# Kernel tuning notes

Hardware: AMD Instinct MI355X
Metric: run time of the kernel (lower is better)

Reference implementation:

```python
import jax, jax.numpy as jnp
import numpy as np

N_NODES = 100000
N_EDGES = 1200000
D = 64
NUM_LAYERS = 3
K = 3


def setup_inputs() -> dict:
    key = jax.random.key(0)
    k1, k2, k3, k4 = jax.random.split(key, 4)
    x = jax.random.normal(k1, (N_NODES, D), dtype=jnp.float32)
    edge_index = jax.random.randint(k2, (2, N_EDGES), 0, N_NODES, dtype=jnp.int64)
    # per-layer Chebyshev linear weights [L, K, in, out] and single bias per layer [L, out]
    W = jax.random.normal(k3, (NUM_LAYERS, K, D, D), dtype=jnp.float32) / np.sqrt(D)
    b = jax.random.normal(k4, (NUM_LAYERS, D), dtype=jnp.float32) * 0.01
    return {"x": x, "edge_index": edge_index, "W": W, "b": b}


def _cheb_norm(edge_index, n_nodes):
    # PyG ChebConv.__norm__ with sym normalization, lambda_max=2.0, no edge weights:
    # scaled Laplacian L_hat = -D^{-1/2} A D^{-1/2} (diagonal cancels to 0).
    row, col = edge_index[0], edge_index[1]
    deg = jax.ops.segment_sum(jnp.ones_like(row, dtype=jnp.float32), row,
                              num_segments=n_nodes)
    deg_inv_sqrt = jnp.where(deg > 0, jax.lax.rsqrt(jnp.maximum(deg, 1.0)), 0.0)
    norm = -deg_inv_sqrt[row] * deg_inv_sqrt[col]  # [E]
    return norm


def _propagate(h, src, dst, norm, n_nodes):
    # out[i] = sum_{e: dst_e = i} norm_e * h[src_e]
    msgs = norm[:, None] * h[src]  # [E, D]
    return jax.ops.segment_sum(msgs, dst, num_segments=n_nodes)


def _cheb_conv(h, src, dst, norm, Wl, bl, n_nodes):
    # Tx_0 = h; Tx_1 = L_hat h; Tx_k = 2 L_hat Tx_{k-1} - Tx_{k-2}
    Tx0 = h
    out = Tx0 @ Wl[0]
    Tx1 = _propagate(Tx0, src, dst, norm, n_nodes)
    out = out + Tx1 @ Wl[1]
    for k in range(2, K):
        Tx2 = 2.0 * _propagate(Tx1, src, dst, norm, n_nodes) - Tx0
        out = out + Tx2 @ Wl[k]
        Tx0, Tx1 = Tx1, Tx2
    return out + bl


def reference(x, edge_index, W, b) -> jnp.ndarray:
    n_nodes = x.shape[0]
    src, dst = edge_index[0], edge_index[1]  # flow source_to_target: j=src, i=dst
    norm = _cheb_norm(edge_index, n_nodes)
    # input_dim == hidden_dim -> no input projection; h_prev starts as x
    h_prev = x
    for i in range(NUM_LAYERS):
        inp = x if i == 0 else h_prev
        out = _cheb_conv(inp, src, dst, norm, W[i], b[i], n_nodes)
        if i > 0:
            out = out + h_prev
        h_prev = jax.nn.relu(out)  # dropout identity in eval mode
    return h_prev
```

## Files before the change

kernel.cpp:

```cpp
#include <hip/hip_runtime.h>

#define N_NODES 100000
#define N_EDGES 1200000
#define D 64
#define NUM_LAYERS 3

#define NB 196
#define BSZ 512
#define NPAD (NB * BSZ)
#define CHUNK 4096
#define NCHUNK ((N_EDGES + CHUNK - 1) / CHUNK)
#define ZROW N_NODES
#define BSLACK 3592

typedef unsigned int uint;
typedef unsigned short u16;

using short8 = __attribute__((ext_vector_type(8))) short;
using f32x4  = __attribute__((ext_vector_type(4))) float;

static __device__ __forceinline__ float b2f(u16 u) {
    return __uint_as_float(((uint)u) << 16);
}
static __device__ __forceinline__ u16 f2b(float f) {
    uint u = __float_as_uint(f);
    return (u16)((u + 0x7FFFu + ((u >> 16) & 1u)) >> 16);
}

__global__ __launch_bounds__(256) void hist_kernel(const int* __restrict__ src,
        const int* __restrict__ dst, int* __restrict__ cnt2, int E) {
    __shared__ int hD[NB], hS[NB];
    for (int i = threadIdx.x; i < NB; i += 256) { hD[i] = 0; hS[i] = 0; }
    __syncthreads();
    int i = blockIdx.x * 256 + threadIdx.x;
    int stride = gridDim.x * 256;
    for (; i < E; i += stride) {
        atomicAdd(&hD[((unsigned)dst[i]) >> 9], 1);
        atomicAdd(&hS[((unsigned)src[i]) >> 9], 1);
    }
    __syncthreads();
    for (int i2 = threadIdx.x; i2 < NB; i2 += 256) {
        if (hD[i2]) atomicAdd(&cnt2[i2], hD[i2]);
        if (hS[i2]) atomicAdd(&cnt2[NB + i2], hS[i2]);
    }
}

__global__ __launch_bounds__(256) void scanb_kernel(const int* __restrict__ cnt2,
        int* __restrict__ base2, int* __restrict__ curs2) {
    __shared__ int buf[256];
    int t = threadIdx.x;
    for (int arr = 0; arr < 2; ++arr) {
        int v = (t < NB) ? cnt2[arr * NB + t] : 0;
        buf[t] = v;
        __syncthreads();
        for (int off = 1; off < 256; off <<= 1) {
            int u = (t >= off) ? buf[t - off] : 0;
            __syncthreads();
            buf[t] += u;
            __syncthreads();
        }
        int excl = buf[t] - v;
        if (t < NB) {
            base2[arr * (NB + 1) + t] = excl;
            curs2[arr * NB + t] = excl;
        }
        if (t == NB - 1) base2[arr * (NB + 1) + NB] = buf[t];
        __syncthreads();
    }
}

__global__ __launch_bounds__(256) void part_kernel(const int* __restrict__ src,
        const int* __restrict__ dst, int* __restrict__ cursD, int* __restrict__ cursS,
        int* __restrict__ dstPart, u16* __restrict__ srcPart, int E) {
    __shared__ int eS[CHUNK], eT[CHUNK];
    __shared__ int hD[NB], hS[NB], bD[NB], bS[NB];
    int e0 = blockIdx.x * CHUNK;
    int n = min(CHUNK, E - e0);
    for (int i = threadIdx.x; i < NB; i += 256) { hD[i] = 0; hS[i] = 0; }
    for (int i = threadIdx.x; i < n; i += 256) { eS[i] = src[e0 + i]; eT[i] = dst[e0 + i]; }
    __syncthreads();
    for (int i = threadIdx.x; i < n; i += 256) {
        atomicAdd(&hD[((unsigned)eT[i]) >> 9], 1);
        atomicAdd(&hS[((unsigned)eS[i]) >> 9], 1);
    }
    __syncthreads();
    for (int i = threadIdx.x; i < NB; i += 256) {
        bD[i] = hD[i] ? atomicAdd(&cursD[i], hD[i]) : 0;
        bS[i] = hS[i] ? atomicAdd(&cursS[i], hS[i]) : 0;
        hD[i] = 0; hS[i] = 0;
    }
    __syncthreads();
    for (int i = threadIdx.x; i < n; i += 256) {
        int s = eS[i], t = eT[i];
        int kb = ((unsigned)t) >> 9;
        int pos = bD[kb] + atomicAdd(&hD[kb], 1);
        dstPart[pos] = ((t & 511) << 20) | s;
        kb = ((unsigned)s) >> 9;
        pos = bS[kb] + atomicAdd(&hS[kb], 1);
        srcPart[pos] = (u16)(s & 511);
    }
}

__global__ __launch_bounds__(256) void csr_kernel(const int* __restrict__ baseD,
        const int* __restrict__ dstPart, int* __restrict__ rowptr,
        int* __restrict__ rowend, int* __restrict__ cv) {
    __shared__ int cnt[BSZ], curs[BSZ], psum[256];
    int b = blockIdx.x, t = threadIdx.x;
    int node0 = b * BSZ;
    int eb = baseD[b], ee = baseD[b + 1];
    int padbase = ((eb + 7) & ~7) + b * BSLACK;
    for (int i = t; i < BSZ; i += 256) cnt[i] = 0;
    __syncthreads();
    for (int e = eb + t; e < ee; e += 256)
        atomicAdd(&cnt[((unsigned)dstPart[e]) >> 20], 1);
    __syncthreads();
    int c0 = cnt[2 * t], c1 = cnt[2 * t + 1];
    int p0 = (c0 + 7) & ~7, p1 = (c1 + 7) & ~7;
    psum[t] = p0 + p1;
    __syncthreads();
    for (int off = 1; off < 256; off <<= 1) {
        int u = (t >= off) ? psum[t - off] : 0;
        __syncthreads();
        psum[t] += u;
        __syncthreads();
    }
    int excl = psum[t] - p0 - p1;
    int start0 = padbase + excl;
    int start1 = start0 + p0;
    curs[2 * t] = start0;
    curs[2 * t + 1] = start1;
    int n0 = node0 + 2 * t;
    if (n0 < N_NODES)     { rowptr[n0]     = start0; rowend[n0]     = start0 + p0; }
    if (n0 + 1 < N_NODES) { rowptr[n0 + 1] = start1; rowend[n0 + 1] = start1 + p1; }
    __syncthreads();
    for (int e = eb + t; e < ee; e += 256) {
        int p = dstPart[e];
        int loc = ((unsigned)p) >> 20;
        int pos = atomicAdd(&curs[loc], 1);
        cv[pos] = p & 0xFFFFF;
    }
    __syncthreads();
    for (int q = c0; q < p0; ++q) cv[start0 + q] = ZROW;
    for (int q = c1; q < p1; ++q) cv[start1 + q] = ZROW;
}

__global__ __launch_bounds__(256) void degs_kernel(const int* __restrict__ baseS,
        const u16* __restrict__ srcPart, float* __restrict__ dinv) {
    __shared__ int cnt[BSZ];
    int b = blockIdx.x, t = threadIdx.x;
    int eb = baseS[b], ee = baseS[b + 1];
    for (int i = t; i < BSZ; i += 256) cnt[i] = 0;
    __syncthreads();
    for (int e = eb + t; e < ee; e += 256)
        atomicAdd(&cnt[srcPart[e]], 1);
    __syncthreads();
    for (int i = t; i < BSZ; i += 256) {
        int node = b * BSZ + i;
        if (node < N_NODES) {
            int d = cnt[i];
            dinv[node] = (d > 0) ? rsqrtf((float)d) : 0.0f;
        }
    }
}

__global__ __launch_bounds__(256) void wprep_kernel(const float* __restrict__ W,
        u16* __restrict__ Wb) {
    int i = blockIdx.x * 256 + threadIdx.x;
    if (i >= 72 * 512) return;
    int j = i & 7;
    int lane = (i >> 3) & 63;
    int fid = i >> 9;
    int ni = fid & 1;
    int t = fid >> 1;
    int kt = t % 6;
    int t2 = t / 6;
    int wn = t2 & 1;
    int l = t2 >> 1;
    int k = kt * 32 + (lane >> 4) * 8 + j;
    int col = wn * 32 + ni * 16 + (lane & 15);
    float v = W[((size_t)l * 192 + k) * 64 + col];
    if (l > 0 && k == col) v += 1.0f;
    Wb[i] = f2b(v);
}

__global__ void zrow_kernel(u16* a, u16* b, u16* c) {
    int i = threadIdx.x;
    if (i >= 192) return;
    u16* buf = (i < 64) ? a : (i < 128) ? b : c;
    buf[(size_t)ZROW * D + (i & 63)] = 0;
}

__global__ __launch_bounds__(256) void cvt_kernel(const float* __restrict__ x,
        const float* __restrict__ dinv, u16* __restrict__ gx, int nvec) {
    int i = blockIdx.x * blockDim.x + threadIdx.x;
    if (i >= nvec) return;
    float4 v = ((const float4*)x)[i];
    float dv = dinv[i >> 4];
    uint2 b;
    b.x = (uint)f2b(v.x * dv) | ((uint)f2b(v.y * dv) << 16);
    b.y = (uint)f2b(v.z * dv) | ((uint)f2b(v.w * dv) << 16);
    ((uint2*)gx)[i] = b;
}

__global__ __launch_bounds__(256) void gather_kernel(const int* __restrict__ rowptr,
        const int* __restrict__ rowend, const int* __restrict__ cv,
        const u16* __restrict__ g, const float* __restrict__ dinv,
        u16* __restrict__ outp, u16* __restrict__ outscaled, int n) {
    int lane = threadIdx.x & 63;
    int node = __builtin_amdgcn_readfirstlane((int)(blockIdx.x * 4) + (threadIdx.x >> 6));
    if (node >= n) return;
    int p = rowptr[node];
    const int pe = rowend[node];
    const int len = pe - p;
    float a0 = 0.f, a1 = 0.f, a2 = 0.f, a3 = 0.f,
          a4 = 0.f, a5 = 0.f, a6 = 0.f, a7 = 0.f;
    if (len == 16) {
        int4 c0 = *(const int4*)(cv + p);
        int4 c1 = *(const int4*)(cv + p + 4);
        int4 c2 = *(const int4*)(cv + p + 8);
        int4 c3 = *(const int4*)(cv + p + 12);
        float v0  = b2f(g[(size_t)c0.x * D + lane]);
        float v1  = b2f(g[(size_t)c0.y * D + lane]);
        float v2  = b2f(g[(size_t)c0.z * D + lane]);
        float v3  = b2f(g[(size_t)c0.w * D + lane]);
        float v4  = b2f(g[(size_t)c1.x * D + lane]);
        float v5  = b2f(g[(size_t)c1.y * D + lane]);
        float v6  = b2f(g[(size_t)c1.z * D + lane]);
        float v7  = b2f(g[(size_t)c1.w * D + lane]);
        float v8  = b2f(g[(size_t)c2.x * D + lane]);
        float v9  = b2f(g[(size_t)c2.y * D + lane]);
        float v10 = b2f(g[(size_t)c2.z * D + lane]);
        float v11 = b2f(g[(size_t)c2.w * D + lane]);
        float v12 = b2f(g[(size_t)c3.x * D + lane]);
        float v13 = b2f(g[(size_t)c3.y * D + lane]);
        float v14 = b2f(g[(size_t)c3.z * D + lane]);
        float v15 = b2f(g[(size_t)c3.w * D + lane]);
        a0 = (v0 + v8);  a1 = (v1 + v9);  a2 = (v2 + v10); a3 = (v3 + v11);
        a4 = (v4 + v12); a5 = (v5 + v13); a6 = (v6 + v14); a7 = (v7 + v15);
    } else if (len > 0) {
        int4 ca = *(const int4*)(cv + p);
        int4 cb = *(const int4*)(cv + p + 4);
        for (;;) {
            int np = p + 8;
            bool more = np < pe;
            int4 na, nb;
            if (more) {
                na = *(const int4*)(cv + np);
                nb = *(const int4*)(cv + np + 4);
            }
            a0 += b2f(g[(size_t)ca.x * D + lane]);
            a1 += b2f(g[(size_t)ca.y * D + lane]);
            a2 += b2f(g[(size_t)ca.z * D + lane]);
            a3 += b2f(g[(size_t)ca.w * D + lane]);
            a4 += b2f(g[(size_t)cb.x * D + lane]);
            a5 += b2f(g[(size_t)cb.y * D + lane]);
            a6 += b2f(g[(size_t)cb.z * D + lane]);
            a7 += b2f(g[(size_t)cb.w * D + lane]);
            if (!more) break;
            ca = na; cb = nb; p = np;
        }
    }
    float dv = dinv[node];
    float v = -dv * (((a0 + a1) + (a2 + a3)) + ((a4 + a5) + (a6 + a7)));
    size_t ob = (size_t)node * D + lane;
    outp[ob] = f2b(v);
    if (outscaled) outscaled[ob] = f2b(dv * v);
}

template<int INPF32>
__global__ __launch_bounds__(256) void cheb_mfma_kernel(
        const float* __restrict__ x,
        const u16* __restrict__ inp,
        const u16* __restrict__ t1, const u16* __restrict__ t2,
        const u16* __restrict__ Wbl,
        const float* __restrict__ bias, const float* __restrict__ dinv,
        u16* __restrict__ outb, u16* __restrict__ goutb, float* __restrict__ outf,
        int writeScaled, int outF32) {
    const int tid = threadIdx.x;
    const int lane = tid & 63;
    const int w = tid >> 6;
    const int wm = w & 1, wn = w >> 1;
    const int l15 = lane & 15;
    const int l4 = lane >> 4;
    const int koff = l4 * 8;

    const int mbase = blockIdx.x * 64 + wm * 32;
    const int nbase = wn * 32;

    short8 Bf[6][2];
#pragma unroll
    for (int kt = 0; kt < 6; ++kt)
#pragma unroll
        for (int ni = 0; ni < 2; ++ni)
            Bf[kt][ni] = *(const short8*)(Wbl + (size_t)(((wn * 6 + kt) * 2) + ni) * 512 + lane * 8);

    short8 T1[2][2], T2[2][2], Fi[2][2];
    float4 Xf[2][2][2];
#pragma unroll
    for (int mi = 0; mi < 2; ++mi) {
        int row = mbase + mi * 16 + l15;
        int rowc = min(row, N_NODES - 1);
#pragma unroll
        for (int half = 0; half < 2; ++half) {
            T1[mi][half] = *(const short8*)(t1 + (size_t)row * 64 + half * 32 + koff);
            T2[mi][half] = *(const short8*)(t2 + (size_t)row * 64 + half * 32 + koff);
            if (INPF32) {
                const float* p = x + (size_t)rowc * 64 + half * 32 + koff;
                Xf[mi][half][0] = *(const float4*)p;
                Xf[mi][half][1] = *(const float4*)(p + 4);
            } else {
                Fi[mi][half] = *(const short8*)(inp + (size_t)row * 64 + half * 32 + koff);
            }
        }
    }

    float bj0 = bias[nbase + l15];
    float bj1 = bias[nbase + 16 + l15];

    f32x4 acc[2][2];
#pragma unroll
    for (int mi = 0; mi < 2; ++mi)
#pragma unroll
        for (int ni = 0; ni < 2; ++ni)
#pragma unroll
            for (int r = 0; r < 4; ++r) acc[mi][ni][r] = 0.0f;

#pragma unroll
    for (int kt = 0; kt < 6; ++kt) {
        short8 Af[2];
#pragma unroll
        for (int mi = 0; mi < 2; ++mi) {
            short8 a;
            if (kt < 2) {
                if (INPF32) {
                    const float* p = (const float*)&Xf[mi][kt][0];
#pragma unroll
                    for (int j = 0; j < 8; ++j) a[j] = (short)f2b(p[j]);
                } else {
                    a = Fi[mi][kt];
                }
            } else if (kt < 4) {
                a = T1[mi][kt - 2];
            } else {
                short8 a2 = T2[mi][kt - 4];
                if (INPF32) {
                    const float* p = (const float*)&Xf[mi][kt - 4][0];
#pragma unroll
                    for (int j = 0; j < 8; ++j)
                        a[j] = (short)f2b(fmaf(2.0f, b2f((u16)a2[j]), -p[j]));
                } else {
                    short8 ai = Fi[mi][kt - 4];
#pragma unroll
                    for (int j = 0; j < 8; ++j)
                        a[j] = (short)f2b(fmaf(2.0f, b2f((u16)a2[j]), -b2f((u16)ai[j])));
                }
            }
            Af[mi] = a;
        }
#pragma unroll
        for (int mi = 0; mi < 2; ++mi)
#pragma unroll
            for (int ni = 0; ni < 2; ++ni)
                acc[mi][ni] = __builtin_amdgcn_mfma_f32_16x16x32_bf16(
                    Af[mi], Bf[kt][ni], acc[mi][ni], 0, 0, 0);
    }

    float4 dvv[2];
    if (writeScaled) {
#pragma unroll
        for (int mi = 0; mi < 2; ++mi)
            dvv[mi] = *(const float4*)(dinv + mbase + mi * 16 + l4 * 4);
    }
#pragma unroll
    for (int mi = 0; mi < 2; ++mi)
#pragma unroll
        for (int r = 0; r < 4; ++r) {
            int node = mbase + mi * 16 + l4 * 4 + r;
            if (node >= N_NODES) continue;
#pragma unroll
            for (int ni = 0; ni < 2; ++ni) {
                int col = nbase + ni * 16 + l15;
                size_t o = (size_t)node * 64 + col;
                float v = acc[mi][ni][r] + (ni ? bj1 : bj0);
                v = fmaxf(v, 0.0f);
                if (outF32) {
                    outf[o] = v;
                } else {
                    outb[o] = f2b(v);
                    if (writeScaled) {
                        float dv = ((const float*)&dvv[mi])[r];
                        goutb[o] = f2b(v * dv);
                    }
                }
            }
        }
}

extern "C" void kernel_launch(void* const* d_in, const int* in_sizes, int n_in,
                              void* d_out, int out_size, void* d_ws, size_t ws_size,
                              hipStream_t stream) {
    const float* x = (const float*)d_in[0];
    const int* ei = (const int*)d_in[1];
    const float* W = (const float*)d_in[2];
    const float* b = (const float*)d_in[3];
    float* out = (float*)d_out;

    const int* src = ei;
    const int* dst = ei + N_EDGES;

    const size_t NDP = (size_t)NPAD * D;
    const size_t CVSZ = (size_t)N_EDGES + 72 + (size_t)NB * BSLACK;

    char* w = (char*)d_ws;
    int*   cnt2   = (int*)w;        w += (size_t)512 * 4;
    int*   base2  = (int*)w;        w += (size_t)512 * 4;
    int*   curs2  = (int*)w;        w += (size_t)512 * 4;
    int*   rowptr = (int*)w;        w += (size_t)NPAD * 4;
    int*   rowend = (int*)w;        w += (size_t)NPAD * 4;
    float* dinv   = (float*)w;      w += (size_t)NPAD * 4;
    u16*   Wb     = (u16*)w;        w += (size_t)72 * 512 * 2;
    int*   cv     = (int*)w;        w += ((CVSZ + 63) & ~(size_t)63) * 4;
    u16*   gx     = (u16*)w;        w += NDP * 2;
    u16*   h      = (u16*)w;        w += NDP * 2;
    u16*   gh     = (u16*)w;        w += NDP * 2;
    u16*   t1     = (u16*)w;        w += NDP * 2;
    u16*   gt1    = (u16*)w;        w += NDP * 2;
    u16*   t2     = (u16*)w;        w += NDP * 2;
    int*   dstPart = (int*)gt1;
    u16*   srcPart = (u16*)t2;

    int* baseD = base2;
    int* baseS = base2 + (NB + 1);
    int* cursD = curs2;
    int* cursS = curs2 + NB;

    hipMemsetAsync(cnt2, 0, (size_t)(2 * NB) * 4, stream);
    hist_kernel<<<304, 256, 0, stream>>>(src, dst, cnt2, N_EDGES);
    scanb_kernel<<<1, 256, 0, stream>>>(cnt2, base2, curs2);
    part_kernel<<<NCHUNK, 256, 0, stream>>>(src, dst, cursD, cursS, dstPart, srcPart, N_EDGES);
    csr_kernel<<<NB, 256, 0, stream>>>(baseD, dstPart, rowptr, rowend, cv);
    degs_kernel<<<NB, 256, 0, stream>>>(baseS, srcPart, dinv);
    wprep_kernel<<<144, 256, 0, stream>>>(W, Wb);
    zrow_kernel<<<1, 256, 0, stream>>>(gx, gh, gt1);
    cvt_kernel<<<(int)(((size_t)N_NODES * D / 4 + 255) / 256), 256, 0, stream>>>(
        x, dinv, gx, (int)((size_t)N_NODES * D / 4));

    const int gatherBlocks = (N_NODES + 3) / 4;
    const int chebBlocks = NPAD / 64;

    for (int l = 0; l < NUM_LAYERS; ++l) {
        const u16* gin = (l == 0) ? gx : gh;
        gather_kernel<<<gatherBlocks, 256, 0, stream>>>(rowptr, rowend, cv, gin, dinv, t1, gt1, N_NODES);
        gather_kernel<<<gatherBlocks, 256, 0, stream>>>(rowptr, rowend, cv, gt1, dinv, t2, (u16*)0, N_NODES);

        int last = (l == NUM_LAYERS - 1);
        const u16* Wbl = Wb + (size_t)l * 24 * 512;
        const float* bl = b + (size_t)l * D;
        if (l == 0) {
            cheb_mfma_kernel<1><<<chebBlocks, 256, 0, stream>>>(
                x, h, t1, t2, Wbl, bl, dinv, h, gh, out, !last, last);
        } else {
            cheb_mfma_kernel<0><<<chebBlocks, 256, 0, stream>>>(
                x, h, t1, t2, Wbl, bl, dinv, h, gh, out, !last, last);
        }
    }
}
```

Measured before the change: 336.0 us.

## Split gathered feature buffers into two 32-column halves for cache-local gathers

Scaled bf16 feature buffers are stored as two separate half-width planes (32 columns each), and the gather kernel now uses twice as many blocks, each handling one half. Within a wave, four 16-lane groups each load a 4-byte pair for a different neighbor, then reduce across groups with shuffles. The goal is to halve the gather working set per pass so it fits better in L2/MALL and to issue wider per-lane loads. The cost is that index lists are read twice, shuffle reductions are added, and the writers (cvt, cheb MFMA output, zrow) must use the new split layout.

```diff
diff --git a/kernel.cpp b/kernel.cpp
--- a/kernel.cpp
+++ b/kernel.cpp
@@ -12,6 +12,7 @@
 #define NCHUNK ((N_EDGES + CHUNK - 1) / CHUNK)
 #define ZROW N_NODES
 #define BSLACK 3592
+#define HSZ ((size_t)NPAD * 32)
 
 typedef unsigned int uint;
 typedef unsigned short u16;
@@ -25,6 +26,12 @@
 static __device__ __forceinline__ u16 f2b(float f) {
     uint u = __float_as_uint(f);
     return (u16)((u + 0x7FFFu + ((u >> 16) & 1u)) >> 16);
+}
+static __device__ __forceinline__ float blo(uint v) {
+    return __uint_as_float(v << 16);
+}
+static __device__ __forceinline__ float bhi(uint v) {
+    return __uint_as_float(v & 0xFFFF0000u);
 }
 
 __global__ __launch_bounds__(256) void hist_kernel(const int* __restrict__ src,
@@ -187,84 +194,95 @@
     int i = threadIdx.x;
     if (i >= 192) return;
     u16* buf = (i < 64) ? a : (i < 128) ? b : c;
-    buf[(size_t)ZROW * D + (i & 63)] = 0;
+    int r = i & 63;
+    int q = r >> 5, fl = r & 31;
+    buf[(size_t)q * HSZ + (size_t)ZROW * 32 + fl] = 0;
 }
 
 __global__ __launch_bounds__(256) void cvt_kernel(const float* __restrict__ x,
-        const float* __restrict__ dinv, u16* __restrict__ gx, int nvec) {
+        const float* __restrict__ dinv, u16* __restrict__ gx2, int nvec) {
     int i = blockIdx.x * blockDim.x + threadIdx.x;
     if (i >= nvec) return;
     float4 v = ((const float4*)x)[i];
-    float dv = dinv[i >> 4];
+    int node = i >> 4;
+    int c = (i & 15) * 4;
+    float dv = dinv[node];
     uint2 b;
     b.x = (uint)f2b(v.x * dv) | ((uint)f2b(v.y * dv) << 16);
     b.y = (uint)f2b(v.z * dv) | ((uint)f2b(v.w * dv) << 16);
-    ((uint2*)gx)[i] = b;
+    *(uint2*)(gx2 + (size_t)(c >> 5) * HSZ + (size_t)node * 32 + (c & 31)) = b;
 }
 
 __global__ __launch_bounds__(256) void gather_kernel(const int* __restrict__ rowptr,
         const int* __restrict__ rowend, const int* __restrict__ cv,
-        const u16* __restrict__ g, const float* __restrict__ dinv,
-        u16* __restrict__ outp, u16* __restrict__ outscaled, int n) {
+        const u16* __restrict__ g2, const float* __restrict__ dinv,
+        u16* __restrict__ trow, u16* __restrict__ gq2, int n) {
+    const int G2 = (N_NODES + 3) / 4;
+    int bid = blockIdx.x;
+    int q = (bid >= G2) ? 1 : 0;
+    int nb = q ? bid - G2 : bid;
     int lane = threadIdx.x & 63;
-    int node = __builtin_amdgcn_readfirstlane((int)(blockIdx.x * 4) + (threadIdx.x >> 6));
+    int li = lane & 15;
+    int grp = lane >> 4;
+    int node = __builtin_amdgcn_readfirstlane(nb * 4 + (threadIdx.x >> 6));
     if (node >= n) return;
+    const u16* __restrict__ gq = g2 + (size_t)q * HSZ;
+
     int p = rowptr[node];
     const int pe = rowend[node];
-    const int len = pe - p;
-    float a0 = 0.f, a1 = 0.f, a2 = 0.f, a3 = 0.f,
-          a4 = 0.f, a5 = 0.f, a6 = 0.f, a7 = 0.f;
-    if (len == 16) {
+    float s0 = 0.f, s1 = 0.f;
+
+#define SEL(c) ((grp == 0) ? (c).x : (grp == 1) ? (c).y : (grp == 2) ? (c).z : (c).w)
+#define LD(s) (*(const uint*)(gq + (size_t)(s) * 32 + li * 2))
+    if (pe - p == 16) {
         int4 c0 = *(const int4*)(cv + p);
         int4 c1 = *(const int4*)(cv + p + 4);
         int4 c2 = *(const int4*)(cv + p + 8);
         int4 c3 = *(const int4*)(cv + p + 12);
-        float v0  = b2f(g[(size_t)c0.x * D + lane]);
-        float v1  = b2f(g[(size_t)c0.y * D + lane]);
-        float v2  = b2f(g[(size_t)c0.z * D + lane]);
-        float v3  = b2f(g[(size_t)c0.w * D + lane]);
-        float v4  = b2f(g[(size_t)c1.x * D + lane]);
-        float v5  = b2f(g[(size_t)c1.y * D + lane]);
-        float v6  = b2f(g[(size_t)c1.z * D + lane]);
-        float v7  = b2f(g[(size_t)c1.w * D + lane]);
-        float v8  = b2f(g[(size_t)c2.x * D + lane]);
-        float v9  = b2f(g[(size_t)c2.y * D + lane]);
-        float v10 = b2f(g[(size_t)c2.z * D + lane]);
-        float v11 = b2f(g[(size_t)c2.w * D + lane]);
-        float v12 = b2f(g[(size_t)c3.x * D + lane]);
-        float v13 = b2f(g[(size_t)c3.y * D + lane]);
-        float v14 = b2f(g[(size_t)c3.z * D + lane]);
-        float v15 = b2f(g[(size_t)c3.w * D + lane]);
-        a0 = (v0 + v8);  a1 = (v1 + v9);  a2 = (v2 + v10); a3 = (v3 + v11);
-        a4 = (v4 + v12); a5 = (v5 + v13); a6 = (v6 + v14); a7 = (v7 + v15);
-    } else if (len > 0) {
+        uint v0 = LD(SEL(c0));
+        uint v1 = LD(SEL(c1));
+        uint v2 = LD(SEL(c2));
+        uint v3 = LD(SEL(c3));
+        s0 = (blo(v0) + blo(v1)) + (blo(v2) + blo(v3));
+        s1 = (bhi(v0) + bhi(v1)) + (bhi(v2) + bhi(v3));
+    } else if (pe > p) {
         int4 ca = *(const int4*)(cv + p);
         int4 cb = *(const int4*)(cv + p + 4);
         for (;;) {
             int np = p + 8;
             bool more = np < pe;
-            int4 na, nb;
+            int4 na, nb4;
             if (more) {
-                na = *(const int4*)(cv + np);
-                nb = *(const int4*)(cv + np + 4);
+                na  = *(const int4*)(cv + np);
+                nb4 = *(const int4*)(cv + np + 4);
             }
-            a0 += b2f(g[(size_t)ca.x * D + lane]);
-            a1 += b2f(g[(size_t)ca.y * D + lane]);
-            a2 += b2f(g[(size_t)ca.z * D + lane]);
-            a3 += b2f(g[(size_t)ca.w * D + lane]);
-            a4 += b2f(g[(size_t)cb.x * D + lane]);
-            a5 += b2f(g[(size_t)cb.y * D + lane]);
-            a6 += b2f(g[(size_t)cb.z * D + lane]);
-            a7 += b2f(g[(size_t)cb.w * D + lane]);
+            uint v0 = LD(SEL(ca));
+            uint v1 = LD(SEL(cb));
+            s0 += blo(v0) + blo(v1);
+            s1 += bhi(v0) + bhi(v1);
             if (!more) break;
-            ca = na; cb = nb; p = np;
-        }
-    }
-    float dv = dinv[node];
-    float v = -dv * (((a0 + a1) + (a2 + a3)) + ((a4 + a5) + (a6 + a7)));
-    size_t ob = (size_t)node * D + lane;
-    outp[ob] = f2b(v);
-    if (outscaled) outscaled[ob] = f2b(dv * v);
+            ca = na; cb = nb4; p = np;
+        }
+    }
+#undef LD
+#undef SEL
+
+    s0 += __shfl_xor(s0, 16);
+    s0 += __shfl_xor(s0, 32);
+    s1 += __shfl_xor(s1, 16);
+    s1 += __shfl_xor(s1, 32);
+
+    if (grp == 0) {
+        float dv = dinv[node];
+        float v0 = -dv * s0;
+        float v1 = -dv * s1;
+        uint pk = (uint)f2b(v0) | ((uint)f2b(v1) << 16);
+        *(uint*)(trow + (size_t)node * 64 + q * 32 + li * 2) = pk;
+        if (gq2) {
+            uint pg = (uint)f2b(dv * v0) | ((uint)f2b(dv * v1) << 16);
+            *(uint*)(gq2 + (size_t)q * HSZ + (size_t)node * 32 + li * 2) = pg;
+        }
+    }
 }
 
 template<int INPF32>
@@ -274,7 +292,7 @@
         const u16* __restrict__ t1, const u16* __restrict__ t2,
         const u16* __restrict__ Wbl,
         const float* __restrict__ bias, const float* __restrict__ dinv,
-        u16* __restrict__ outb, u16* __restrict__ goutb, float* __restrict__ outf,
+        u16* __restrict__ outb, u16* __restrict__ goutb2, float* __restrict__ outf,
         int writeScaled, int outF32) {
     const int tid = threadIdx.x;
     const int lane = tid & 63;
@@ -389,7 +407,8 @@
                     outb[o] = f2b(v);
                     if (writeScaled) {
                         float dv = ((const float*)&dvv[mi])[r];
-                        goutb[o] = f2b(v * dv);
+                        goutb2[(size_t)wn * HSZ + (size_t)node * 32 + (col & 31)] =
+                            f2b(v * dv);
                     }
                 }
             }
@@ -445,7 +464,8 @@
     cvt_kernel<<<(int)(((size_t)N_NODES * D / 4 + 255) / 256), 256, 0, stream>>>(
         x, dinv, gx, (int)((size_t)N_NODES * D / 4));
 
-    const int gatherBlocks = (N_NODES + 3) / 4;
+    const int G2 = (N_NODES + 3) / 4;
+    const int gatherBlocks = 2 * G2;
     const int chebBlocks = NPAD / 64;
 
     for (int l = 0; l < NUM_LAYERS; ++l) {
```

Measured after the change: 482.2 us. 43.5% more time.

## Keep Chebyshev features in degree-scaled space to drop dual outputs

Applied to the files above, without the earlier changes.

Stores all intermediate features pre-multiplied by D^{-1/2}, so each gather writes a single scaled output (scaled by -1/deg) instead of both raw and scaled copies. The MFMA kernel reads only scaled buffers and rescales accumulators by sqrt(deg) in the epilogue, which removes the fp32 x load path and the second output write. This cuts memory traffic in the gather and combine kernels. Isolated nodes use a scale of 1 to stay correct, and rescaling bf16 values can change rounding.

```diff
diff --git a/kernel.cpp b/kernel.cpp
--- a/kernel.cpp
+++ b/kernel.cpp
@@ -145,7 +145,8 @@
 }
 
 __global__ __launch_bounds__(256) void degs_kernel(const int* __restrict__ baseS,
-        const u16* __restrict__ srcPart, float* __restrict__ dinv) {
+        const u16* __restrict__ srcPart, float* __restrict__ sArr,
+        float* __restrict__ rsArr, float* __restrict__ mArr) {
     __shared__ int cnt[BSZ];
     int b = blockIdx.x, t = threadIdx.x;
     int eb = baseS[b], ee = baseS[b + 1];
@@ -158,7 +159,10 @@
         int node = b * BSZ + i;
         if (node < N_NODES) {
             int d = cnt[i];
-            dinv[node] = (d > 0) ? rsqrtf((float)d) : 0.0f;
+            float fd = (float)d;
+            sArr[node]  = (d > 0) ? rsqrtf(fd) : 1.0f;
+            rsArr[node] = (d > 0) ? sqrtf(fd) : 1.0f;
+            mArr[node]  = (d > 0) ? (-1.0f / fd) : 0.0f;
         }
     }
 }
@@ -191,21 +195,21 @@
 }
 
 __global__ __launch_bounds__(256) void cvt_kernel(const float* __restrict__ x,
-        const float* __restrict__ dinv, u16* __restrict__ gx, int nvec) {
+        const float* __restrict__ sArr, u16* __restrict__ g0, int nvec) {
     int i = blockIdx.x * blockDim.x + threadIdx.x;
     if (i >= nvec) return;
     float4 v = ((const float4*)x)[i];
-    float dv = dinv[i >> 4];
+    float dv = sArr[i >> 4];
     uint2 b;
     b.x = (uint)f2b(v.x * dv) | ((uint)f2b(v.y * dv) << 16);
     b.y = (uint)f2b(v.z * dv) | ((uint)f2b(v.w * dv) << 16);
-    ((uint2*)gx)[i] = b;
+    ((uint2*)g0)[i] = b;
 }
 
 __global__ __launch_bounds__(256) void gather_kernel(const int* __restrict__ rowptr,
         const int* __restrict__ rowend, const int* __restrict__ cv,
-        const u16* __restrict__ g, const float* __restrict__ dinv,
-        u16* __restrict__ outp, u16* __restrict__ outscaled, int n) {
+        const u16* __restrict__ g, const float* __restrict__ mArr,
+        u16* __restrict__ outg, int n) {
     int lane = threadIdx.x & 63;
     int node = __builtin_amdgcn_readfirstlane((int)(blockIdx.x * 4) + (threadIdx.x >> 6));
     if (node >= n) return;
@@ -260,22 +264,16 @@
             ca = na; cb = nb; p = np;
         }
     }
-    float dv = dinv[node];
-    float v = -dv * (((a0 + a1) + (a2 + a3)) + ((a4 + a5) + (a6 + a7)));
-    size_t ob = (size_t)node * D + lane;
-    outp[ob] = f2b(v);
-    if (outscaled) outscaled[ob] = f2b(dv * v);
-}
-
-template<int INPF32>
+    float val = mArr[node] * (((a0 + a1) + (a2 + a3)) + ((a4 + a5) + (a6 + a7)));
+    outg[(size_t)node * D + lane] = f2b(val);
+}
+
 __global__ __launch_bounds__(256) void cheb_mfma_kernel(
-        const float* __restrict__ x,
-        const u16* __restrict__ inp,
-        const u16* __restrict__ t1, const u16* __restrict__ t2,
-        const u16* __restrict__ Wbl,
-        const float* __restrict__ bias, const float* __restrict__ dinv,
-        u16* __restrict__ outb, u16* __restrict__ goutb, float* __restrict__ outf,
-        int writeScaled, int outF32) {
+        const u16* __restrict__ gin, const u16* __restrict__ gt1,
+        const u16* __restrict__ gt2, const u16* __restrict__ Wbl,
+        const float* __restrict__ bias, const float* __restrict__ rsArr,
+        const float* __restrict__ sArr,
+        u16* __restrict__ outg, float* __restrict__ outf, int last) {
     const int tid = threadIdx.x;
     const int lane = tid & 63;
     const int w = tid >> 6;
@@ -294,23 +292,16 @@
         for (int ni = 0; ni < 2; ++ni)
             Bf[kt][ni] = *(const short8*)(Wbl + (size_t)(((wn * 6 + kt) * 2) + ni) * 512 + lane * 8);
 
-    short8 T1[2][2], T2[2][2], Fi[2][2];
-    float4 Xf[2][2][2];
+    short8 G[2][2], T1[2][2], T2[2][2];
 #pragma unroll
     for (int mi = 0; mi < 2; ++mi) {
         int row = mbase + mi * 16 + l15;
-        int rowc = min(row, N_NODES - 1);
 #pragma unroll
         for (int half = 0; half < 2; ++half) {
-            T1[mi][half] = *(const short8*)(t1 + (size_t)row * 64 + half * 32 + koff);
-            T2[mi][half] = *(const short8*)(t2 + (size_t)row * 64 + half * 32 + koff);
-            if (INPF32) {
-                const float* p = x + (size_t)rowc * 64 + half * 32 + koff;
-                Xf[mi][half][0] = *(const float4*)p;
-                Xf[mi][half][1] = *(const float4*)(p + 4);
-            } else {
-                Fi[mi][half] = *(const short8*)(inp + (size_t)row * 64 + half * 32 + koff);
-            }
+            size_t off = (size_t)row * 64 + half * 32 + koff;
+            G[mi][half]  = *(const short8*)(gin + off);
+            T1[mi][half] = *(const short8*)(gt1 + off);
+            T2[mi][half] = *(const short8*)(gt2 + off);
         }
     }
 
@@ -332,28 +323,15 @@
         for (int mi = 0; mi < 2; ++mi) {
             short8 a;
             if (kt < 2) {
-                if (INPF32) {
-                    const float* p = (const float*)&Xf[mi][kt][0];
-#pragma unroll
-                    for (int j = 0; j < 8; ++j) a[j] = (short)f2b(p[j]);
-                } else {
-                    a = Fi[mi][kt];
-                }
+                a = G[mi][kt];
             } else if (kt < 4) {
                 a = T1[mi][kt - 2];
             } else {
                 short8 a2 = T2[mi][kt - 4];
-                if (INPF32) {
-                    const float* p = (const float*)&Xf[mi][kt - 4][0];
-#pragma unroll
-                    for (int j = 0; j < 8; ++j)
-                        a[j] = (short)f2b(fmaf(2.0f, b2f((u16)a2[j]), -p[j]));
-                } else {
-                    short8 ai = Fi[mi][kt - 4];
-#pragma unroll
-                    for (int j = 0; j < 8; ++j)
-                        a[j] = (short)f2b(fmaf(2.0f, b2f((u16)a2[j]), -b2f((u16)ai[j])));
-                }
+                short8 ai = G[mi][kt - 4];
+#pragma unroll
+                for (int j = 0; j < 8; ++j)
+                    a[j] = (short)f2b(fmaf(2.0f, b2f((u16)a2[j]), -b2f((u16)ai[j])));
             }
             Af[mi] = a;
         }
@@ -365,11 +343,11 @@
                     Af[mi], Bf[kt][ni], acc[mi][ni], 0, 0, 0);
     }
 
-    float4 dvv[2];
-    if (writeScaled) {
-#pragma unroll
-        for (int mi = 0; mi < 2; ++mi)
-            dvv[mi] = *(const float4*)(dinv + mbase + mi * 16 + l4 * 4);
+    float4 rsv[2], sv[2];
+#pragma unroll
+    for (int mi = 0; mi < 2; ++mi) {
+        rsv[mi] = *(const float4*)(rsArr + mbase + mi * 16 + l4 * 4);
+        if (!last) sv[mi] = *(const float4*)(sArr + mbase + mi * 16 + l4 * 4);
     }
 #pragma unroll
     for (int mi = 0; mi < 2; ++mi)
@@ -377,20 +355,18 @@
         for (int r = 0; r < 4; ++r) {
             int node = mbase + mi * 16 + l4 * 4 + r;
             if (node >= N_NODES) continue;
+            float rsr = ((const float*)&rsv[mi])[r];
 #pragma unroll
             for (int ni = 0; ni < 2; ++ni) {
                 int col = nbase + ni * 16 + l15;
                 size_t o = (size_t)node * 64 + col;
-                float v = acc[mi][ni][r] + (ni ? bj1 : bj0);
+                float v = fmaf(rsr, acc[mi][ni][r], (ni ? bj1 : bj0));
                 v = fmaxf(v, 0.0f);
-                if (outF32) {
+                if (last) {
                     outf[o] = v;
                 } else {
-                    outb[o] = f2b(v);
-                    if (writeScaled) {
-                        float dv = ((const float*)&dvv[mi])[r];
-                        goutb[o] = f2b(v * dv);
-                    }
+                    float sr = ((const float*)&sv[mi])[r];
+                    outg[o] = f2b(v * sr);
                 }
             }
         }
@@ -417,17 +393,17 @@
     int*   curs2  = (int*)w;        w += (size_t)512 * 4;
     int*   rowptr = (int*)w;        w += (size_t)NPAD * 4;
     int*   rowend = (int*)w;        w += (size_t)NPAD * 4;
-    float* dinv   = (float*)w;      w += (size_t)NPAD * 4;
+    float* sArr   = (float*)w;      w += (size_t)NPAD * 4;
+    float* rsArr  = (float*)w;      w += (size_t)NPAD * 4;
+    float* mArr   = (float*)w;      w += (size_t)NPAD * 4;
     u16*   Wb     = (u16*)w;        w += (size_t)72 * 512 * 2;
     int*   cv     = (int*)w;        w += ((CVSZ + 63) & ~(size_t)63) * 4;
-    u16*   gx     = (u16*)w;        w += NDP * 2;
-    u16*   h      = (u16*)w;        w += NDP * 2;
-    u16*   gh     = (u16*)w;        w += NDP * 2;
-    u16*   t1     = (u16*)w;        w += NDP * 2;
+    u16*   gA     = (u16*)w;        w += NDP * 2;
+    u16*   gB     = (u16*)w;        w += NDP * 2;
     u16*   gt1    = (u16*)w;        w += NDP * 2;
-    u16*   t2     = (u16*)w;        w += NDP * 2;
-    int*   dstPart = (int*)gt1;
-    u16*   srcPart = (u16*)t2;
+    u16*   gt2    = (u16*)w;        w += NDP * 2;
+    int*   dstPart = (int*)gt2;
+    u16*   srcPart = (u16*)gB;
 
     int* baseD = base2;
     int* baseS = base2 + (NB + 1);
@@ -439,29 +415,25 @@
     scanb_kernel<<<1, 256, 0, stream>>>(cnt2, base2, curs2);
     part_kernel<<<NCHUNK, 256, 0, stream>>>(src, dst, cursD, cursS, dstPart, srcPart, N_EDGES);
     csr_kernel<<<NB, 256, 0, stream>>>(baseD, dstPart, rowptr, rowend, cv);
-    degs_kernel<<<NB, 256, 0, stream>>>(baseS, srcPart, dinv);
+    degs_kernel<<<NB, 256, 0, stream>>>(baseS, srcPart, sArr, rsArr, mArr);
     wprep_kernel<<<144, 256, 0, stream>>>(W, Wb);
-    zrow_kernel<<<1, 256, 0, stream>>>(gx, gh, gt1);
+    zrow_kernel<<<1, 256, 0, stream>>>(gA, gB, gt1);
     cvt_kernel<<<(int)(((size_t)N_NODES * D / 4 + 255) / 256), 256, 0, stream>>>(
-        x, dinv, gx, (int)((size_t)N_NODES * D / 4));
+        x, sArr, gA, (int)((size_t)N_NODES * D / 4));
 
     const int gatherBlocks = (N_NODES + 3) / 4;
     const int chebBlocks = NPAD / 64;
 
+    const u16* gin = gA;
     for (int l = 0; l < NUM_LAYERS; ++l) {
-        const u16* gin = (l == 0) ? gx : gh;
-        gather_kernel<<<gatherBlocks, 256, 0, stream>>>(rowptr, rowend, cv, gin, dinv, t1, gt1, N_NODES);
-        gather_kernel<<<gatherBlocks, 256, 0, stream>>>(rowptr, rowend, cv, gt1, dinv, t2, (u16*)0, N_NODES);
+        gather_kernel<<<gatherBlocks, 256, 0, stream>>>(rowptr, rowend, cv, gin, mArr, gt1, N_NODES);
+        gather_kernel<<<gatherBlocks, 256, 0, stream>>>(rowptr, rowend, cv, gt1, mArr, gt2, N_NODES);
 
         int last = (l == NUM_LAYERS - 1);
-        const u16* Wbl = Wb + (size_t)l * 24 * 512;
-        const float* bl = b + (size_t)l * D;
-        if (l == 0) {
-            cheb_mfma_kernel<1><<<chebBlocks, 256, 0, stream>>>(
-                x, h, t1, t2, Wbl, bl, dinv, h, gh, out, !last, last);
-        } else {
-            cheb_mfma_kernel<0><<<chebBlocks, 256, 0, stream>>>(
-                x, h, t1, t2, Wbl, bl, dinv, h, gh, out, !last, last);
-        }
-    }
-}
+        u16* gout = (l == 0) ? gB : gA;
+        cheb_mfma_kernel<<<chebBlocks, 256, 0, stream>>>(
+            gin, gt1, gt2, Wb + (size_t)l * 24 * 512, b + (size_t)l * D,
+            rsArr, sArr, gout, out, last);
+        gin = gout;
+    }
+}
```

New measurement: 326.4 us. -2.9%, faster.
